# Optimization experiments

Hardware: AMD Instinct MI355X
Metric: run time of the kernel (lower is better)

## Reference

```python
import jax, jax.numpy as jnp
import numpy as np

B, S, D, H = 2, 2048, 1024, 16
DK = D // H
DFF = 4 * D
EPS = 1e-6


def layer_norm(x, gamma, beta):
    mu = jnp.mean(x, axis=-1, keepdims=True)
    var = jnp.mean(jnp.square(x - mu), axis=-1, keepdims=True)
    return (x - mu) * jax.lax.rsqrt(var + EPS) * gamma + beta


def setup_inputs() -> dict:
    key = jax.random.key(0)
    ks = jax.random.split(key, 10)
    xavier = (6.0 / (D + D)) ** 0.5
    kaiming = (6.0 / D) ** 0.5
    kaiming2 = (6.0 / DFF) ** 0.5
    return {
        "batch_X": jax.random.normal(ks[0], (B, S, D), dtype=jnp.float32),
        "padding_mask": jax.random.randint(ks[1], (B, S), 0, 2, dtype=jnp.int32),
        "W_Q": jax.random.uniform(ks[2], (D, D), jnp.float32, -xavier, xavier),
        "W_K": jax.random.uniform(ks[3], (D, D), jnp.float32, -xavier, xavier),
        "W_V": jax.random.uniform(ks[4], (D, D), jnp.float32, -xavier, xavier),
        "W_O": jax.random.uniform(ks[5], (D, D), jnp.float32, -xavier, xavier),
        "W1": jax.random.uniform(ks[6], (D, DFF), jnp.float32, -kaiming, kaiming),
        "b1": jnp.zeros((DFF,), jnp.float32),
        "W2": jax.random.uniform(ks[7], (DFF, D), jnp.float32, -kaiming2, kaiming2),
        "b2": jnp.zeros((D,), jnp.float32),
        "gamma1": jnp.ones((D,), jnp.float32),
        "beta1": jnp.zeros((D,), jnp.float32),
        "gamma2": jnp.ones((D,), jnp.float32),
        "beta2": jnp.zeros((D,), jnp.float32),
    }


def reference(batch_X, padding_mask, W_Q, W_K, W_V, W_O, W1, b1, W2, b2,
              gamma1, beta1, gamma2, beta2):
    x = batch_X
    b, s, d = x.shape

    # --- multi-head self-attention (use_mask=False: padding mask only) ---
    q = (x @ W_Q).reshape(b, s, H, DK)
    k = (x @ W_K).reshape(b, s, H, DK)
    v = (x @ W_V).reshape(b, s, H, DK)
    scores = jnp.einsum("bqhd,bkhd->bhqk", q, k) / jnp.sqrt(jnp.float32(DK))
    # mask[b,i,j] = (padding_mask[b,i] == 0) for all j: whole query rows are
    # either fully masked (softmax -> NaN -> zeroed in the original) or
    # fully unmasked. Equivalent math: softmax then zero padded query rows.
    probs = jax.nn.softmax(scores, axis=-1)
    keep = (padding_mask != 0).astype(probs.dtype)[:, None, :, None]  # [B,1,S,1]
    probs = probs * keep
    ctx = jnp.einsum("bhqk,bkhd->bqhd", probs, v).reshape(b, s, d)
    attn_out = ctx @ W_O

    # --- residual + LN (dropout identity in eval) ---
    x = x + layer_norm(attn_out, gamma1, beta1)

    # --- FFN ---
    h = jax.nn.relu(x @ W1 + b1)
    ffn_out = h @ W2 + b2
    x = x + layer_norm(ffn_out, gamma2, beta2)
    return x
```

## Files before the change

kernel.cpp:

```cpp
#include <hip/hip_runtime.h>
#include <hip/hip_bf16.h>

#define B 2
#define S 2048
#define D 1024
#define H 16
#define DKh 64
#define DFF 4096
#define M (B*S)

typedef unsigned short u16;
typedef unsigned int u32;
typedef __attribute__((ext_vector_type(8))) short short8;
typedef __attribute__((ext_vector_type(4))) float f32x4;

__device__ __forceinline__ u16 f2bf(float f) {
  union { float f; unsigned u; } v; v.f = f;
  unsigned r = v.u + 0x7fffu + ((v.u >> 16) & 1u);
  return (u16)(r >> 16);
}

__device__ __forceinline__ float bf2f(u16 h) {
  union { u32 u; float f; } v; v.u = ((u32)h) << 16; return v.f;
}

__device__ __forceinline__ u32 pkbf2(float a, float b) {
  __hip_bfloat162 h = __float22bfloat162_rn(make_float2(a, b));
  return *reinterpret_cast<u32*>(&h);
}

__device__ __forceinline__ void gload16(const void* g, void* l) {
  __builtin_amdgcn_global_load_lds((const __attribute__((address_space(1))) void*)g,
                                   (__attribute__((address_space(3))) void*)l, 16, 0, 0);
}

#define SBAR()  __builtin_amdgcn_sched_barrier(0)
#define WBAR()  __builtin_amdgcn_s_barrier()

__global__ __launch_bounds__(256) void cvtbf(const float* __restrict__ in,
                                             u16* __restrict__ out, int n4) {
  int i = blockIdx.x * 256 + threadIdx.x;
  if (i >= n4) return;
  float4 v = ((const float4*)in)[i];
  ushort4 o = make_ushort4(f2bf(v.x), f2bf(v.y), f2bf(v.z), f2bf(v.w));
  ((ushort4*)out)[i] = o;
}

__global__ __launch_bounds__(256) void tcvt4(const float* __restrict__ Wq,
    const float* __restrict__ Wk, const float* __restrict__ Wv,
    const float* __restrict__ Wo, u16* __restrict__ dQKV, u16* __restrict__ dO) {
  __shared__ u16 l[64][65];
  const int z = blockIdx.z;
  const float* W = (z == 0) ? Wq : (z == 1) ? Wk : (z == 2) ? Wv : Wo;
  u16* Wt = (z < 3) ? dQKV + (size_t)z * D * D : dO;
  const int n0 = blockIdx.x * 64, k0 = blockIdx.y * 64;
  const int tx = threadIdx.x & 63, ty = threadIdx.x >> 6;
#pragma unroll
  for (int j = 0; j < 16; ++j) {
    int r = j * 4 + ty;
    l[r][tx] = f2bf(W[(size_t)(k0 + r) * D + n0 + tx]);
  }
  __syncthreads();
#pragma unroll
  for (int j = 0; j < 16; ++j) {
    int r = j * 4 + ty;
    Wt[(size_t)(n0 + r) * D + k0 + tx] = l[tx][r];
  }
}

__global__ __launch_bounds__(256) void tcvt(const float* __restrict__ W,
                                            u16* __restrict__ Wt, int K, int N) {
  __shared__ u16 l[64][65];
  const int n0 = blockIdx.x * 64, k0 = blockIdx.y * 64;
  const int tx = threadIdx.x & 63, ty = threadIdx.x >> 6;
#pragma unroll
  for (int j = 0; j < 16; ++j) {
    int r = j * 4 + ty;
    l[r][tx] = f2bf(W[(size_t)(k0 + r) * N + n0 + tx]);
  }
  __syncthreads();
#pragma unroll
  for (int j = 0; j < 16; ++j) {
    int r = j * 4 + ty;
    Wt[(size_t)(n0 + r) * K + k0 + tx] = l[tx][r];
  }
}

__global__ __launch_bounds__(256) void vtrans(const u16* __restrict__ V,
                                              u16* __restrict__ Vt, int ld) {
  __shared__ u16 l[64][65];
  const int s0 = blockIdx.x * 64, by = blockIdx.y;
  const int b = by >> 4, h = by & 15;
  const int tx = threadIdx.x & 63, ty = threadIdx.x >> 6;
#pragma unroll
  for (int j = 0; j < 16; ++j) {
    int r = j * 4 + ty;
    l[r][tx] = V[(size_t)(b * S + s0 + r) * ld + h * DKh + tx];
  }
  __syncthreads();
#pragma unroll
  for (int j = 0; j < 16; ++j) {
    int r = j * 4 + ty;
    Vt[(size_t)(by * 64 + r) * S + s0 + tx] = l[tx][r];
  }
}

template<int EPI>
__global__ __launch_bounds__(512, 2) void gemm256(const u16* __restrict__ Ag,
    const u16* __restrict__ Bg, void* __restrict__ Cout,
    const float* __restrict__ bias, int Mm, int N, int ld, int Kper,
    int sCols, float qscl) {
  __shared__ u16 lA[2 * 16384];
  __shared__ u16 lB[2 * 16384];
  const int t = threadIdx.x;
  const int lane = t & 63, w = t >> 6;
  const int wm = w >> 2, wn = w & 3;
  const int g = lane >> 4, c = lane & 15;
  const int swz = (c & 7) << 4;

  const int gx = gridDim.x, gy = gridDim.y;
  const int orig = blockIdx.y * gx + blockIdx.x;
  const int qchunk = (gx * gy) >> 3;
  const int wg = (orig & 7) * qchunk + (orig >> 3);
  const int bn0 = (wg % gx) * 256, bm0 = (wg / gx) * 256;
  const int koff = blockIdx.z * Kper;
  const int nk = Kper >> 6;

  f32x4 acc[8][4] = {};
  short8 af[4][2], bf[2][2];

  auto stageA = [&](int h, int buf, int kt) {
#pragma unroll
    for (int i = 0; i < 2; ++i) {
      int chunk = i * 512 + t;
      int rh = chunk >> 3;
      int cb = (chunk & 7) * 16;
      int r = (rh & 63) + (h + 2 * (rh >> 6)) * 64;
      gload16(Ag + (size_t)(bm0 + r) * ld + koff + kt * 64 + ((cb ^ ((r & 7) << 4)) >> 1),
              (void*)((char*)lA + buf * 32768 + h * 16384 + chunk * 16));
    }
  };
  auto stageB = [&](int h, int buf, int kt) {
#pragma unroll
    for (int i = 0; i < 2; ++i) {
      int chunk = i * 512 + t;
      int rh = chunk >> 3;
      int cb = (chunk & 7) * 16;
      int r = (rh & 31) + (h + 2 * (rh >> 5)) * 32;
      gload16(Bg + (size_t)(bn0 + r) * ld + koff + kt * 64 + ((cb ^ ((r & 7) << 4)) >> 1),
              (void*)((char*)lB + buf * 32768 + h * 16384 + chunk * 16));
    }
  };

#define RDA(mh) { const char* lab = (const char*)lA + cur * 32768;                          \
  _Pragma("unroll") for (int mt2 = 0; mt2 < 4; ++mt2)                                       \
    _Pragma("unroll") for (int kc = 0; kc < 2; ++kc)                                        \
      af[mt2][kc] = *(const short8*)(lab + (wm * 64 + (mh) * 128 + mt2 * 16 + c) * 128      \
                                         + ((kc * 64 + g * 16) ^ swz)); }
#define RDB(nh) { const char* lbb = (const char*)lB + cur * 32768;                          \
  _Pragma("unroll") for (int nt2 = 0; nt2 < 2; ++nt2)                                       \
    _Pragma("unroll") for (int kc = 0; kc < 2; ++kc)                                        \
      bf[nt2][kc] = *(const short8*)(lbb + ((nh) * 128 + wn * 32 + nt2 * 16 + c) * 128      \
                                         + ((kc * 64 + g * 16) ^ swz)); }
#define QMFMA(mh, nh) { __builtin_amdgcn_s_setprio(1);                                      \
  _Pragma("unroll") for (int mt2 = 0; mt2 < 4; ++mt2)                                       \
    _Pragma("unroll") for (int nt2 = 0; nt2 < 2; ++nt2)                                     \
      _Pragma("unroll") for (int kc = 0; kc < 2; ++kc)                                      \
        acc[(mh) * 4 + mt2][(nh) * 2 + nt2] = __builtin_amdgcn_mfma_f32_16x16x32_bf16(      \
            af[mt2][kc], bf[nt2][kc], acc[(mh) * 4 + mt2][(nh) * 2 + nt2], 0, 0, 0);        \
  __builtin_amdgcn_s_setprio(0); }

  stageA(0, 0, 0); stageB(0, 0, 0); stageA(1, 0, 0); stageB(1, 0, 0);
  asm volatile("s_waitcnt vmcnt(4)" ::: "memory");
  SBAR(); WBAR(); SBAR();

  int cur = 0;
  for (int kt = 0; kt < nk; ++kt) {
    const bool more = (kt + 1 < nk);
    RDB(0); RDA(0);
    if (more) { stageA(0, cur ^ 1, kt + 1);
                asm volatile("s_waitcnt vmcnt(4)" ::: "memory"); }
    else      { asm volatile("s_waitcnt vmcnt(2)" ::: "memory"); }
    SBAR(); WBAR(); SBAR();
    QMFMA(0, 0);
    SBAR(); WBAR(); SBAR();
    RDA(1);
    if (more) { stageB(0, cur ^ 1, kt + 1);
                asm volatile("s_waitcnt vmcnt(4)" ::: "memory"); }
    else      { asm volatile("s_waitcnt vmcnt(0)" ::: "memory"); }
    SBAR(); WBAR(); SBAR();
    QMFMA(1, 0);
    SBAR(); WBAR(); SBAR();
    RDB(1);
    if (more) stageA(1, cur ^ 1, kt + 1);
    SBAR(); WBAR(); SBAR();
    QMFMA(1, 1);
    SBAR(); WBAR(); SBAR();
    RDA(0);
    if (more) { stageB(1, cur ^ 1, kt + 1);
                asm volatile("s_waitcnt vmcnt(4)" ::: "memory"); }
    SBAR(); WBAR(); SBAR();
    QMFMA(0, 1);
    SBAR(); WBAR(); SBAR();
    cur ^= 1;
  }
#undef RDA
#undef RDB
#undef QMFMA

  float* plane = (EPI == 1) ? ((float*)Cout + (size_t)blockIdx.z * Mm * N) : (float*)Cout;
#pragma unroll
  for (int mt = 0; mt < 8; ++mt) {
#pragma unroll
    for (int nt = 0; nt < 4; ++nt) {
      const int col = bn0 + wn * 64 + nt * 16 + c;
      float bv = (EPI == 2) ? bias[col] : 0.0f;
#pragma unroll
      for (int r = 0; r < 4; ++r) {
        const int row = bm0 + wm * 128 + mt * 16 + g * 4 + r;
        float v = acc[mt][nt][r];
        if (EPI == 2) v = fmaxf(v + bv, 0.0f);
        if (EPI == 0 && col < sCols) v *= qscl;
        if (EPI == 1) plane[(size_t)row * N + col] = v;
        else          ((u16*)Cout)[(size_t)row * N + col] = f2bf(v);
      }
    }
  }
}

__global__ __launch_bounds__(256) void attn_kernel(const u16* __restrict__ Q,
    const u16* __restrict__ Kp, const u16* __restrict__ Vt,
    const int* __restrict__ mask, u16* __restrict__ Ctx, int ldq) {
  __shared__ u16 lK[2][64 * 64];
  __shared__ u16 lV[2][64 * 64];
  __shared__ u16 lP[4 * 16 * 64];
  const int t = threadIdx.x, lane = t & 63, w = t >> 6;
  const int g = lane >> 4, c = lane & 15;
  const int gx = gridDim.x;
  const int orig = blockIdx.y * gx + blockIdx.x;
  const int qchunk = (gx * gridDim.y) >> 3;
  const int wg = (orig & 7) * qchunk + (orig >> 3);
  const int bx = wg % gx, by = wg / gx;
  const int b = by >> 4, h = by & 15;
  const int q0w = bx * 64 + w * 16;

  short8 qf[2];
#pragma unroll
  for (int kc = 0; kc < 2; ++kc)
    qf[kc] = *(const short8*)&Q[(size_t)(b * S + q0w + c) * ldq + h * DKh + kc * 32 + g * 8];

  float lsum = 0.0f;
  f32x4 accO[4] = {};

  auto stage = [&](int buf, int it) {
    const int kv0 = it * 64;
#pragma unroll
    for (int q = 0; q < 2; ++q) {
      int idx = q * 256 + t;
      int row = idx >> 3;
      int colb = (idx & 7) * 16;
      int scol = colb ^ ((row & 7) << 4);
      gload16(Kp + (size_t)(b * S + kv0 + row) * ldq + h * DKh + scol / 2,
              (void*)(&lK[buf][0] + idx * 8));
      gload16(Vt + (size_t)(by * 64 + row) * S + kv0 + scol / 2,
              (void*)(&lV[buf][0] + idx * 8));
    }
  };

  stage(0, 0);
  int cur = 0;
  for (int it = 0; it < S / 64; ++it) {
    __syncthreads();
    if (it + 1 < S / 64) stage(cur ^ 1, it + 1);

    f32x4 sc[4];
#pragma unroll
    for (int ct = 0; ct < 4; ++ct) {
      f32x4 z = {0.f, 0.f, 0.f, 0.f};
#pragma unroll
      for (int kc = 0; kc < 2; ++kc) {
        int row = ct * 16 + c;
        int bcol = (kc * 64 + g * 16) ^ ((row & 7) << 4);
        short8 kf = *(const short8*)&lK[cur][row * 64 + bcol / 2];
        z = __builtin_amdgcn_mfma_f32_16x16x32_bf16(kf, qf[kc], z, 0, 0, 0);
      }
      sc[ct] = z;
    }

#pragma unroll
    for (int ct = 0; ct < 4; ++ct) {
      float p0 = __builtin_amdgcn_exp2f(sc[ct][0]);
      float p1 = __builtin_amdgcn_exp2f(sc[ct][1]);
      float p2 = __builtin_amdgcn_exp2f(sc[ct][2]);
      float p3 = __builtin_amdgcn_exp2f(sc[ct][3]);
      lsum += (p0 + p1) + (p2 + p3);
      uint2 pk;
      pk.x = pkbf2(p0, p1);
      pk.y = pkbf2(p2, p3);
      *(uint2*)&lP[w * 1024 + c * 64 + (((ct * 32 + g * 8) ^ ((c & 7) << 4)) >> 1)] = pk;
    }

    short8 pa[2];
#pragma unroll
    for (int kc = 0; kc < 2; ++kc)
      pa[kc] = *(const short8*)&lP[w * 1024 + c * 64 + (((kc * 64 + g * 16) ^ ((c & 7) << 4)) >> 1)];
#pragma unroll
    for (int dt = 0; dt < 4; ++dt) {
#pragma unroll
      for (int kc = 0; kc < 2; ++kc) {
        int rowV = dt * 16 + c;
        int bcolV = (kc * 64 + g * 16) ^ ((rowV & 7) << 4);
        short8 vb = *(const short8*)&lV[cur][rowV * 64 + bcolV / 2];
        accO[dt] = __builtin_amdgcn_mfma_f32_16x16x32_bf16(pa[kc], vb, accO[dt], 0, 0, 0);
      }
    }
    cur ^= 1;
  }

  lsum += __shfl_xor(lsum, 16);
  lsum += __shfl_xor(lsum, 32);

#pragma unroll
  for (int r = 0; r < 4; ++r) {
    int qrow = g * 4 + r;
    float lq = __shfl(lsum, qrow);
    int q = q0w + qrow;
    int keep = mask[b * S + q];
    float inv = (keep != 0) ? (1.0f / lq) : 0.0f;
#pragma unroll
    for (int dt = 0; dt < 4; ++dt) {
      float o = accO[dt][r] * inv;
      Ctx[(size_t)(b * S + q) * D + h * DKh + dt * 16 + c] = f2bf(o);
    }
  }
}

__global__ __launch_bounds__(256) void ln_res(const float* __restrict__ planes,
    int np, const float* __restrict__ bias, const float* __restrict__ XresF,
    const u16* __restrict__ XresB, const float* __restrict__ gamma,
    const float* __restrict__ beta, float* __restrict__ outF,
    u16* __restrict__ outB) {
  __shared__ float s1[4], s2[4];
  const int row = blockIdx.x, t = threadIdx.x;
  float4 y = ((const float4*)(planes + (size_t)row * D))[t];
  for (int j = 1; j < np; ++j) {
    const float4 y2 = ((const float4*)(planes + (size_t)j * M * D + (size_t)row * D))[t];
    y.x += y2.x; y.y += y2.y; y.z += y2.z; y.w += y2.w;
  }
  if (bias) {
    const float4 bb = ((const float4*)bias)[t];
    y.x += bb.x; y.y += bb.y; y.z += bb.z; y.w += bb.w;
  }
  float sm = y.x + y.y + y.z + y.w;
  float sq = y.x * y.x + y.y * y.y + y.z * y.z + y.w * y.w;
#pragma unroll
  for (int m2 = 1; m2 <= 32; m2 <<= 1) { sm += __shfl_xor(sm, m2); sq += __shfl_xor(sq, m2); }
  if ((t & 63) == 0) { s1[t >> 6] = sm; s2[t >> 6] = sq; }
  __syncthreads();
  float tot = s1[0] + s1[1] + s1[2] + s1[3];
  float tsq = s2[0] + s2[1] + s2[2] + s2[3];
  float mu = tot * (1.0f / D);
  float var = tsq * (1.0f / D) - mu * mu;
  float rstd = rsqrtf(var + 1e-6f);
  float4 xr;
  if (XresF) {
    xr = ((const float4*)(XresF + (size_t)row * D))[t];
  } else {
    ushort4 xb = ((const ushort4*)(XresB + (size_t)row * D))[t];
    xr.x = bf2f(xb.x); xr.y = bf2f(xb.y); xr.z = bf2f(xb.z); xr.w = bf2f(xb.w);
  }
  const float4 ga = ((const float4*)gamma)[t];
  const float4 be = ((const float4*)beta)[t];
  float4 o;
  o.x = xr.x + (y.x - mu) * rstd * ga.x + be.x;
  o.y = xr.y + (y.y - mu) * rstd * ga.y + be.y;
  o.z = xr.z + (y.z - mu) * rstd * ga.z + be.z;
  o.w = xr.w + (y.w - mu) * rstd * ga.w + be.w;
  if (outF) ((float4*)(outF + (size_t)row * D))[t] = o;
  if (outB) {
    ushort4 ob = make_ushort4(f2bf(o.x), f2bf(o.y), f2bf(o.z), f2bf(o.w));
    ((ushort4*)outB)[(size_t)row * (D / 4) + t] = ob;
  }
}

extern "C" void kernel_launch(void* const* d_in, const int* in_sizes, int n_in,
                              void* d_out, int out_size, void* d_ws, size_t ws_size,
                              hipStream_t stream) {
  const float* X   = (const float*)d_in[0];
  const int*   msk = (const int*)d_in[1];
  const float* WQ  = (const float*)d_in[2];
  const float* WK  = (const float*)d_in[3];
  const float* WV  = (const float*)d_in[4];
  const float* WO  = (const float*)d_in[5];
  const float* W1  = (const float*)d_in[6];
  const float* b1  = (const float*)d_in[7];
  const float* W2  = (const float*)d_in[8];
  const float* b2  = (const float*)d_in[9];
  const float* g1  = (const float*)d_in[10];
  const float* be1 = (const float*)d_in[11];
  const float* g2  = (const float*)d_in[12];
  const float* be2 = (const float*)d_in[13];
  float* out = (float*)d_out;
  const float SCL = 0.18033688011112042f;

  char* ws = (char*)d_ws;
  size_t off = 0;
  auto alloc = [&](size_t bytes) {
    void* p = ws + off;
    off += (bytes + 1023) & ~(size_t)1023;
    return p;
  };
  u16* Xb     = (u16*)alloc((size_t)M * D * 2);
  u16* WQKVt  = (u16*)alloc((size_t)3 * D * D * 2);
  u16* WOt    = (u16*)alloc((size_t)D * D * 2);
  u16* W1t    = (u16*)alloc((size_t)DFF * D * 2);
  u16* W2t    = (u16*)alloc((size_t)D * DFF * 2);
  u16* QKVb   = (u16*)alloc((size_t)M * 3 * D * 2);
  u16* Vt     = (u16*)alloc((size_t)B * H * DKh * S * 2);
  u16* Ctx    = (u16*)alloc((size_t)M * D * 2);
  u16* X1b    = (u16*)alloc((size_t)M * D * 2);
  u16* Hb     = (u16*)alloc((size_t)M * DFF * 2);
  float* PP   = (float*)QKVb;
  if (off > ws_size) return;
  size_t off4 = off;
  float* PP4 = (float*)(ws + off4);
  off4 += (size_t)4 * M * D * 4;
  const bool split4 = (off4 <= ws_size);

  dim3 blk(256), blk5(512);

  cvtbf<<<dim3(M * D / 4 / 256), blk, 0, stream>>>(X, Xb, M * D / 4);
  tcvt4<<<dim3(D / 64, D / 64, 4), blk, 0, stream>>>(WQ, WK, WV, WO, WQKVt, WOt);
  tcvt<<<dim3(DFF / 64, D / 64), blk, 0, stream>>>(W1, W1t, D, DFF);
  tcvt<<<dim3(D / 64, DFF / 64), blk, 0, stream>>>(W2, W2t, DFF, D);
  gemm256<0><<<dim3(3 * D / 256, M / 256), blk5, 0, stream>>>(Xb, WQKVt, QKVb, nullptr, M, 3 * D, D, D, D, SCL);
  vtrans<<<dim3(S / 64, B * H), blk, 0, stream>>>(QKVb + 2 * D, Vt, 3 * D);
  attn_kernel<<<dim3(S / 64, B * H), blk, 0, stream>>>(QKVb, QKVb + D, Vt, msk, Ctx, 3 * D);
  gemm256<1><<<dim3(D / 256, M / 256, 2), blk5, 0, stream>>>(Ctx, WOt, PP, nullptr, M, D, D, D / 2, 0, 1.0f);
  ln_res<<<dim3(M), blk, 0, stream>>>(PP, 2, nullptr, X, nullptr, g1, be1, nullptr, X1b);
  gemm256<2><<<dim3(DFF / 256, M / 256), blk5, 0, stream>>>(X1b, W1t, Hb, b1, M, DFF, D, D, 0, 1.0f);
  if (split4) {
    gemm256<1><<<dim3(D / 256, M / 256, 4), blk5, 0, stream>>>(Hb, W2t, PP4, nullptr, M, D, DFF, DFF / 4, 0, 1.0f);
    ln_res<<<dim3(M), blk, 0, stream>>>(PP4, 4, b2, nullptr, X1b, g2, be2, out, nullptr);
  } else {
    gemm256<1><<<dim3(D / 256, M / 256, 2), blk5, 0, stream>>>(Hb, W2t, PP, nullptr, M, D, DFF, DFF / 2, 0, 1.0f);
    ln_res<<<dim3(M), blk, 0, stream>>>(PP, 2, b2, nullptr, X1b, g2, be2, out, nullptr);
  }
}
```

Measured before the change: 254.6 us.

## Enlarge attention query tile to 256 rows and merge prep conversions into one kernel

The attention kernel now has each wave handle four 16-row query sub-tiles (256 queries per block), so each staged K/V tile in LDS is reused four times. This cuts global K/V traffic and the per-tile barrier overhead. The cost is much higher register use (16 accumulators, 8 Q fragments), a larger P buffer in LDS, and only 256 blocks, which may reduce occupancy. Separately, the four preprocessing launches (X cast and weight transpose-converts) are merged into one kernel to save launch overhead.

```diff
diff --git a/kernel.cpp b/kernel.cpp
--- a/kernel.cpp
+++ b/kernel.cpp
@@ -37,41 +37,8 @@
 #define SBAR()  __builtin_amdgcn_sched_barrier(0)
 #define WBAR()  __builtin_amdgcn_s_barrier()
 
-__global__ __launch_bounds__(256) void cvtbf(const float* __restrict__ in,
-                                             u16* __restrict__ out, int n4) {
-  int i = blockIdx.x * 256 + threadIdx.x;
-  if (i >= n4) return;
-  float4 v = ((const float4*)in)[i];
-  ushort4 o = make_ushort4(f2bf(v.x), f2bf(v.y), f2bf(v.z), f2bf(v.w));
-  ((ushort4*)out)[i] = o;
-}
-
-__global__ __launch_bounds__(256) void tcvt4(const float* __restrict__ Wq,
-    const float* __restrict__ Wk, const float* __restrict__ Wv,
-    const float* __restrict__ Wo, u16* __restrict__ dQKV, u16* __restrict__ dO) {
-  __shared__ u16 l[64][65];
-  const int z = blockIdx.z;
-  const float* W = (z == 0) ? Wq : (z == 1) ? Wk : (z == 2) ? Wv : Wo;
-  u16* Wt = (z < 3) ? dQKV + (size_t)z * D * D : dO;
-  const int n0 = blockIdx.x * 64, k0 = blockIdx.y * 64;
-  const int tx = threadIdx.x & 63, ty = threadIdx.x >> 6;
-#pragma unroll
-  for (int j = 0; j < 16; ++j) {
-    int r = j * 4 + ty;
-    l[r][tx] = f2bf(W[(size_t)(k0 + r) * D + n0 + tx]);
-  }
-  __syncthreads();
-#pragma unroll
-  for (int j = 0; j < 16; ++j) {
-    int r = j * 4 + ty;
-    Wt[(size_t)(n0 + r) * D + k0 + tx] = l[tx][r];
-  }
-}
-
-__global__ __launch_bounds__(256) void tcvt(const float* __restrict__ W,
-                                            u16* __restrict__ Wt, int K, int N) {
-  __shared__ u16 l[64][65];
-  const int n0 = blockIdx.x * 64, k0 = blockIdx.y * 64;
+__device__ __forceinline__ void tcvt_body(const float* __restrict__ W,
+    u16* __restrict__ Wt, int K, int N, int n0, int k0, u16 (*l)[65]) {
   const int tx = threadIdx.x & 63, ty = threadIdx.x >> 6;
 #pragma unroll
   for (int j = 0; j < 16; ++j) {
@@ -83,6 +50,34 @@
   for (int j = 0; j < 16; ++j) {
     int r = j * 4 + ty;
     Wt[(size_t)(n0 + r) * K + k0 + tx] = l[tx][r];
+  }
+}
+
+__global__ __launch_bounds__(256) void prep(const float* __restrict__ X,
+    u16* __restrict__ Xb, const float* __restrict__ Wq, const float* __restrict__ Wk,
+    const float* __restrict__ Wv, const float* __restrict__ Wo,
+    u16* __restrict__ dQKV, u16* __restrict__ dO,
+    const float* __restrict__ W1, u16* __restrict__ W1t,
+    const float* __restrict__ W2, u16* __restrict__ W2t) {
+  __shared__ u16 l[64][65];
+  const int bid = blockIdx.x;
+  if (bid < 4096) {
+    int i = bid * 256 + threadIdx.x;
+    float4 v = ((const float4*)X)[i];
+    ushort4 o = make_ushort4(f2bf(v.x), f2bf(v.y), f2bf(v.z), f2bf(v.w));
+    ((ushort4*)Xb)[i] = o;
+  } else if (bid < 5120) {
+    int bid2 = bid - 4096;
+    int z = bid2 >> 8, r2 = bid2 & 255;
+    const float* W = (z == 0) ? Wq : (z == 1) ? Wk : (z == 2) ? Wv : Wo;
+    u16* Wt = (z < 3) ? dQKV + (size_t)z * D * D : dO;
+    tcvt_body(W, Wt, D, D, (r2 & 15) * 64, (r2 >> 4) * 64, l);
+  } else if (bid < 6144) {
+    int r2 = bid - 5120;
+    tcvt_body(W1, W1t, D, DFF, (r2 & 63) * 64, (r2 >> 6) * 64, l);
+  } else {
+    int r2 = bid - 6144;
+    tcvt_body(W2, W2t, DFF, D, (r2 & 15) * 64, (r2 >> 4) * 64, l);
   }
 }
 
@@ -233,7 +228,7 @@
     const int* __restrict__ mask, u16* __restrict__ Ctx, int ldq) {
   __shared__ u16 lK[2][64 * 64];
   __shared__ u16 lV[2][64 * 64];
-  __shared__ u16 lP[4 * 16 * 64];
+  __shared__ u16 lP[4 * 4 * 1024];
   const int t = threadIdx.x, lane = t & 63, w = t >> 6;
   const int g = lane >> 4, c = lane & 15;
   const int gx = gridDim.x;
@@ -242,15 +237,17 @@
   const int wg = (orig & 7) * qchunk + (orig >> 3);
   const int bx = wg % gx, by = wg / gx;
   const int b = by >> 4, h = by & 15;
-  const int q0w = bx * 64 + w * 16;
-
-  short8 qf[2];
-#pragma unroll
-  for (int kc = 0; kc < 2; ++kc)
-    qf[kc] = *(const short8*)&Q[(size_t)(b * S + q0w + c) * ldq + h * DKh + kc * 32 + g * 8];
-
-  float lsum = 0.0f;
-  f32x4 accO[4] = {};
+  const int q0w = bx * 256 + w * 16;
+
+  short8 qf[4][2];
+#pragma unroll
+  for (int s = 0; s < 4; ++s)
+#pragma unroll
+    for (int kc = 0; kc < 2; ++kc)
+      qf[s][kc] = *(const short8*)&Q[(size_t)(b * S + q0w + s * 64 + c) * ldq + h * DKh + kc * 32 + g * 8];
+
+  float lsum[4] = {0.f, 0.f, 0.f, 0.f};
+  f32x4 accO[4][4] = {};
 
   auto stage = [&](int buf, int it) {
     const int kv0 = it * 64;
@@ -273,37 +270,35 @@
     __syncthreads();
     if (it + 1 < S / 64) stage(cur ^ 1, it + 1);
 
-    f32x4 sc[4];
 #pragma unroll
     for (int ct = 0; ct < 4; ++ct) {
-      f32x4 z = {0.f, 0.f, 0.f, 0.f};
-#pragma unroll
-      for (int kc = 0; kc < 2; ++kc) {
-        int row = ct * 16 + c;
-        int bcol = (kc * 64 + g * 16) ^ ((row & 7) << 4);
-        short8 kf = *(const short8*)&lK[cur][row * 64 + bcol / 2];
-        z = __builtin_amdgcn_mfma_f32_16x16x32_bf16(kf, qf[kc], z, 0, 0, 0);
+      int row = ct * 16 + c;
+      short8 kf0 = *(const short8*)&lK[cur][row * 64 + (((0 * 64 + g * 16) ^ ((row & 7) << 4)) >> 1)];
+      short8 kf1 = *(const short8*)&lK[cur][row * 64 + (((1 * 64 + g * 16) ^ ((row & 7) << 4)) >> 1)];
+#pragma unroll
+      for (int s = 0; s < 4; ++s) {
+        f32x4 z = {0.f, 0.f, 0.f, 0.f};
+        z = __builtin_amdgcn_mfma_f32_16x16x32_bf16(kf0, qf[s][0], z, 0, 0, 0);
+        z = __builtin_amdgcn_mfma_f32_16x16x32_bf16(kf1, qf[s][1], z, 0, 0, 0);
+        float p0 = __builtin_amdgcn_exp2f(z[0]);
+        float p1 = __builtin_amdgcn_exp2f(z[1]);
+        float p2 = __builtin_amdgcn_exp2f(z[2]);
+        float p3 = __builtin_amdgcn_exp2f(z[3]);
+        lsum[s] += (p0 + p1) + (p2 + p3);
+        uint2 pk;
+        pk.x = pkbf2(p0, p1);
+        pk.y = pkbf2(p2, p3);
+        *(uint2*)&lP[(w * 4 + s) * 1024 + c * 64 + (((ct * 32 + g * 8) ^ ((c & 7) << 4)) >> 1)] = pk;
       }
-      sc[ct] = z;
-    }
-
-#pragma unroll
-    for (int ct = 0; ct < 4; ++ct) {
-      float p0 = __builtin_amdgcn_exp2f(sc[ct][0]);
-      float p1 = __builtin_amdgcn_exp2f(sc[ct][1]);
-      float p2 = __builtin_amdgcn_exp2f(sc[ct][2]);
-      float p3 = __builtin_amdgcn_exp2f(sc[ct][3]);
-      lsum += (p0 + p1) + (p2 + p3);
-      uint2 pk;
-      pk.x = pkbf2(p0, p1);
-      pk.y = pkbf2(p2, p3);
-      *(uint2*)&lP[w * 1024 + c * 64 + (((ct * 32 + g * 8) ^ ((c & 7) << 4)) >> 1)] = pk;
-    }
-
-    short8 pa[2];
-#pragma unroll
-    for (int kc = 0; kc < 2; ++kc)
-      pa[kc] = *(const short8*)&lP[w * 1024 + c * 64 + (((kc * 64 + g * 16) ^ ((c & 7) << 4)) >> 1)];
+    }
+
+    short8 pa[4][2];
+#pragma unroll
+    for (int s = 0; s < 4; ++s)
+#pragma unroll
+      for (int kc = 0; kc < 2; ++kc)
+        pa[s][kc] = *(const short8*)&lP[(w * 4 + s) * 1024 + c * 64 + (((kc * 64 + g * 16) ^ ((c & 7) << 4)) >> 1)];
+
 #pragma unroll
     for (int dt = 0; dt < 4; ++dt) {
 #pragma unroll
@@ -311,26 +306,31 @@
         int rowV = dt * 16 + c;
         int bcolV = (kc * 64 + g * 16) ^ ((rowV & 7) << 4);
         short8 vb = *(const short8*)&lV[cur][rowV * 64 + bcolV / 2];
-        accO[dt] = __builtin_amdgcn_mfma_f32_16x16x32_bf16(pa[kc], vb, accO[dt], 0, 0, 0);
+#pragma unroll
+        for (int s = 0; s < 4; ++s)
+          accO[s][dt] = __builtin_amdgcn_mfma_f32_16x16x32_bf16(pa[s][kc], vb, accO[s][dt], 0, 0, 0);
       }
     }
     cur ^= 1;
   }
 
-  lsum += __shfl_xor(lsum, 16);
-  lsum += __shfl_xor(lsum, 32);
+#pragma unroll
+  for (int s = 0; s < 4; ++s) {
+    lsum[s] += __shfl_xor(lsum[s], 16);
+    lsum[s] += __shfl_xor(lsum[s], 32);
+  }
 
 #pragma unroll
   for (int r = 0; r < 4; ++r) {
     int qrow = g * 4 + r;
-    float lq = __shfl(lsum, qrow);
-    int q = q0w + qrow;
-    int keep = mask[b * S + q];
-    float inv = (keep != 0) ? (1.0f / lq) : 0.0f;
-#pragma unroll
-    for (int dt = 0; dt < 4; ++dt) {
-      float o = accO[dt][r] * inv;
-      Ctx[(size_t)(b * S + q) * D + h * DKh + dt * 16 + c] = f2bf(o);
+#pragma unroll
+    for (int s = 0; s < 4; ++s) {
+      float lq = __shfl(lsum[s], qrow);
+      int q = q0w + s * 64 + qrow;
+      float inv = (mask[b * S + q] != 0) ? (1.0f / lq) : 0.0f;
+#pragma unroll
+      for (int dt = 0; dt < 4; ++dt)
+        Ctx[(size_t)(b * S + q) * D + h * DKh + dt * 16 + c] = f2bf(accO[s][dt][r] * inv);
     }
   }
 }
@@ -429,13 +429,10 @@
 
   dim3 blk(256), blk5(512);
 
-  cvtbf<<<dim3(M * D / 4 / 256), blk, 0, stream>>>(X, Xb, M * D / 4);
-  tcvt4<<<dim3(D / 64, D / 64, 4), blk, 0, stream>>>(WQ, WK, WV, WO, WQKVt, WOt);
-  tcvt<<<dim3(DFF / 64, D / 64), blk, 0, stream>>>(W1, W1t, D, DFF);
-  tcvt<<<dim3(D / 64, DFF / 64), blk, 0, stream>>>(W2, W2t, DFF, D);
+  prep<<<dim3(7168), blk, 0, stream>>>(X, Xb, WQ, WK, WV, WO, WQKVt, WOt, W1, W1t, W2, W2t);
   gemm256<0><<<dim3(3 * D / 256, M / 256), blk5, 0, stream>>>(Xb, WQKVt, QKVb, nullptr, M, 3 * D, D, D, D, SCL);
   vtrans<<<dim3(S / 64, B * H), blk, 0, stream>>>(QKVb + 2 * D, Vt, 3 * D);
-  attn_kernel<<<dim3(S / 64, B * H), blk, 0, stream>>>(QKVb, QKVb + D, Vt, msk, Ctx, 3 * D);
+  attn_kernel<<<dim3(S / 256, B * H), blk, 0, stream>>>(QKVb, QKVb + D, Vt, msk, Ctx, 3 * D);
   gemm256<1><<<dim3(D / 256, M / 256, 2), blk5, 0, stream>>>(Ctx, WOt, PP, nullptr, M, D, D, D / 2, 0, 1.0f);
   ln_res<<<dim3(M), blk, 0, stream>>>(PP, 2, nullptr, X, nullptr, g1, be1, nullptr, X1b);
   gemm256<2><<<dim3(DFF / 256, M / 256), blk5, 0, stream>>>(X1b, W1t, Hb, b1, M, DFF, D, D, 0, 1.0f);
```

New measurement: 252.2 us. About the same (-1.0%).
